# Kernel tuning notes

Hardware: AMD Instinct MI355X
Metric: run time of the kernel (lower is better)

Reference implementation:

```python
import jax, jax.numpy as jnp
import numpy as np

HEADS = 8
HID = 256
D = HID // HEADS
NEG_SLOPE = 0.2  # PyG leaky_relu negative_slope default in HANConv
NA, NPAP, CIN = 10000, 20000, 256
E = 256000
OUT = 16


def seg_softmax(scores, seg, num_segments):
    # scores: [E, H]; softmax over edges sharing the same dst segment id
    m = jax.ops.segment_max(scores, seg, num_segments=num_segments)
    m = jnp.where(jnp.isfinite(m), m, 0.0)
    e = jnp.exp(scores - m[seg])
    s = jax.ops.segment_sum(e, seg, num_segments=num_segments)
    return e / (s[seg] + 1e-16)


def han_edge(h_src, h_dst, att_src, att_dst, src, dst, num_dst):
    # h_src: [Ns, H, D]; att_*: [H, D]; src/dst: [E]
    a = (h_src * att_src).sum(-1)[src] + (h_dst * att_dst).sum(-1)[dst]  # [E, H]
    alpha = seg_softmax(jax.nn.leaky_relu(a, NEG_SLOPE), dst, num_dst)
    out = jax.ops.segment_sum(h_src[src] * alpha[..., None], dst, num_segments=num_dst)
    return jax.nn.relu(out.reshape(num_dst, HID))


def semantic_group(xs, q, k_W, k_b):
    out = jnp.stack(xs)                                            # [M, N, F]
    score = (jnp.tanh(out @ k_W + k_b) * q).sum(-1).mean(axis=1)   # [M]
    attn = jax.nn.softmax(score)                                   # softmax over metapaths
    return (out * attn[:, None, None]).sum(0)                      # [N, F]


def setup_inputs() -> dict:
    key = jax.random.key(0)
    ks = jax.random.split(key, 32)
    n = lambda i, shape, s: jax.random.normal(ks[i], shape, dtype=jnp.float32) * s
    ri = lambda i, hi: jax.random.randint(ks[i], (E,), 0, hi).astype(jnp.int64)
    w_scale = (1.0 / CIN) ** 0.5
    return {
        "x_author": n(0, (NA, CIN), 1.0),
        "x_paper": n(1, (NPAP, CIN), 1.0),
        "W_author": n(2, (CIN, HID), w_scale),
        "b_author": jnp.zeros((HID,), jnp.float32),
        "W_paper": n(3, (CIN, HID), w_scale),
        "b_paper": jnp.zeros((HID,), jnp.float32),
        "att_sw": n(4, (HEADS, D), 0.1),
        "att_dw": n(5, (HEADS, D), 0.1),
        "att_sc": n(6, (HEADS, D), 0.1),
        "att_dc": n(7, (HEADS, D), 0.1),
        "att_sr": n(8, (HEADS, D), 0.1),
        "att_dr": n(9, (HEADS, D), 0.1),
        "k_W": n(10, (HID, HID), (1.0 / HID) ** 0.5),
        "k_b": jnp.zeros((HID,), jnp.float32),
        "q": n(11, (HID,), 0.1),
        "lin_W": n(12, (HID, OUT), (1.0 / HID) ** 0.5),
        "lin_b": jnp.zeros((OUT,), jnp.float32),
        "ew_src": ri(13, NA), "ew_dst": ri(14, NPAP),
        "ec_src": ri(15, NPAP), "ec_dst": ri(16, NPAP),
        "er_src": ri(17, NPAP), "er_dst": ri(18, NA),
    }


def reference(x_author, x_paper, W_author, b_author, W_paper, b_paper,
              att_sw, att_dw, att_sc, att_dc, att_sr, att_dr,
              k_W, k_b, q, lin_W, lin_b,
              ew_src, ew_dst, ec_src, ec_dst, er_src, er_dst):
    # per-node-type projection -> [N, H, D]
    h_a = (x_author @ W_author + b_author).reshape(NA, HEADS, D)
    h_p = (x_paper @ W_paper + b_paper).reshape(NPAP, HEADS, D)
    # per-edge-type gather / attention / segment-softmax / scatter
    o_writes = han_edge(h_a, h_p, att_sw, att_dw, ew_src, ew_dst, NPAP)  # author->paper
    o_cites = han_edge(h_p, h_p, att_sc, att_dc, ec_src, ec_dst, NPAP)   # paper->paper
    o_rev = han_edge(h_p, h_a, att_sr, att_dr, er_src, er_dst, NA)       # paper->author
    # semantic-level attention over metapaths per dst node type
    paper_out = semantic_group([o_writes, o_cites], q, k_W, k_b)
    author_out = semantic_group([o_rev], q, k_W, k_b)
    # global_add_pool per node type (batch=None -> single graph) + shared linear
    pooled = jnp.stack([author_out.sum(0), paper_out.sum(0)])  # [2, HID]
    return pooled @ lin_W + lin_b                              # [2, OUT]
```

## Files before the change

### kernel.cpp

```cpp
#include <hip/hip_runtime.h>
#include <hip/hip_bf16.h>

#define HEADS 8
#define HID 256
#define NA 10000
#define NPAP 20000
#define NE 256000
#define N_SEG (2 * NPAP + NA)
#define TOTE (3 * NE)
#define NEG_SLOPE 0.2f

typedef __attribute__((ext_vector_type(8))) short bf16x8;
typedef __attribute__((ext_vector_type(4))) float f32x4;

__device__ __forceinline__ short f2bf(float x) {
    unsigned u = __float_as_uint(x);
    unsigned r = (u + 0x7fffu + ((u >> 16) & 1u)) >> 16;
    return (short)r;
}
__device__ __forceinline__ float bf2f(short s) {
    return __uint_as_float(((unsigned)(unsigned short)s) << 16);
}
__device__ __forceinline__ float bflo(unsigned u) { return __uint_as_float(u << 16); }
__device__ __forceinline__ float bfhi(unsigned u) { return __uint_as_float(u & 0xffff0000u); }

#define W_BLKS 48
#define DEG_BLKS 3000
__global__ __launch_bounds__(256) void prep(
    const float* __restrict__ W_a, short* __restrict__ WaT,
    const float* __restrict__ W_p, short* __restrict__ WpT,
    const float* __restrict__ k_W, short* __restrict__ kWT,
    const int* __restrict__ ewd, const int* __restrict__ ecd, const int* __restrict__ erd,
    int* __restrict__ deg4, unsigned short* __restrict__ rank16)
{
    __shared__ short T[64][65];
    int b = blockIdx.x;
    int t = threadIdx.x;
    if (b < W_BLKS) {
        int z = b >> 4, rem = b & 15;
        int k0 = (rem & 3) * 64, c0 = (rem >> 2) * 64;
        const float* W = z == 0 ? W_a : (z == 1 ? W_p : k_W);
        short* Wt      = z == 0 ? WaT : (z == 1 ? WpT : kWT);
        int rr = t >> 6, c = t & 63;
#pragma unroll
        for (int p = 0; p < 16; ++p) {
            int r = rr + p * 4;
            T[c][r] = f2bf(W[(size_t)(k0 + r) * 256 + c0 + c]);
        }
        __syncthreads();
#pragma unroll
        for (int p = 0; p < 16; ++p) {
            int cc = rr + p * 4;
            Wt[(size_t)(c0 + cc) * 256 + k0 + c] = T[cc][c];
        }
    } else {
        int bb = b - W_BLKS;
        int e = bb * 256 + t;
        if (e >= TOTE) return;
        int d;
        if (e < NE)          d = ewd[e];
        else if (e < 2 * NE) d = ecd[e - NE] + NPAP;
        else                 d = erd[e - 2 * NE] + 2 * NPAP;
        int r = atomicAdd(&deg4[(bb & 3) * N_SEG + d], 1);
        rank16[e] = (unsigned short)r;
    }
}

__global__ __launch_bounds__(256) void proj_gemm(
    const float* __restrict__ A0, const short* __restrict__ Wt0, const float* __restrict__ b0,
    short* __restrict__ C0, unsigned char* __restrict__ H80, int N0, int nb0,
    const float* __restrict__ A1, const short* __restrict__ Wt1, const float* __restrict__ b1,
    short* __restrict__ C1, unsigned char* __restrict__ H81, int N1)
{
    __shared__ short As[64][64];
    __shared__ short Ws[256][64];

    int bx = blockIdx.x;
    const float* A; const short* Wt; const float* bias; short* Cb; unsigned char* H8; int N, row0;
    if (bx < nb0) { A = A0; Wt = Wt0; bias = b0; Cb = C0; H8 = H80; N = N0; row0 = bx * 64; }
    else          { A = A1; Wt = Wt1; bias = b1; Cb = C1; H8 = H81; N = N1; row0 = (bx - nb0) * 64; }

    int tid = threadIdx.x;
    int w = tid >> 6, l = tid & 63;
    int lr = l & 15, lh = l >> 4;
    int swz = (l & 7) << 3;

    f32x4 acc[4][4] = {};

    for (int k0 = 0; k0 < 256; k0 += 64) {
#pragma unroll
        for (int i = 0; i < 4; ++i) {
            int lin = tid + i * 256;
            int r = lin >> 4, fc = (lin & 15) << 2;
            float4 v = make_float4(0.f, 0.f, 0.f, 0.f);
            int gr = row0 + r;
            if (gr < N) v = *reinterpret_cast<const float4*>(&A[(size_t)gr * 256 + k0 + fc]);
            short4 o;
            o.x = f2bf(v.x); o.y = f2bf(v.y); o.z = f2bf(v.z); o.w = f2bf(v.w);
            *reinterpret_cast<short4*>(&As[r][fc ^ ((r & 7) << 3)]) = o;
        }
#pragma unroll
        for (int i = 0; i < 8; ++i) {
            int lin = tid + i * 256;
            int c = lin >> 3, kc = (lin & 7) << 3;
            *reinterpret_cast<bf16x8*>(&Ws[c][kc ^ ((c & 7) << 3)]) =
                *reinterpret_cast<const bf16x8*>(&Wt[(size_t)c * 256 + k0 + kc]);
        }
        __syncthreads();
#pragma unroll
        for (int kk = 0; kk < 64; kk += 32) {
            int krow = (kk + lh * 8) ^ swz;
            bf16x8 af[4], bfr[4];
#pragma unroll
            for (int mi = 0; mi < 4; ++mi)
                af[mi] = *reinterpret_cast<bf16x8*>(&As[mi * 16 + lr][krow]);
#pragma unroll
            for (int ni = 0; ni < 4; ++ni)
                bfr[ni] = *reinterpret_cast<bf16x8*>(&Ws[w * 64 + ni * 16 + lr][krow]);
#pragma unroll
            for (int mi = 0; mi < 4; ++mi)
#pragma unroll
                for (int ni = 0; ni < 4; ++ni)
                    acc[mi][ni] = __builtin_amdgcn_mfma_f32_16x16x32_bf16(
                        af[mi], bfr[ni], acc[mi][ni], 0, 0, 0);
        }
        __syncthreads();
    }

#pragma unroll
    for (int mi = 0; mi < 4; ++mi) {
        int rb = row0 + mi * 16 + lh * 4;
#pragma unroll
        for (int ni = 0; ni < 4; ++ni) {
            int c = w * 64 + ni * 16 + lr;
            float bc = bias[c];
#pragma unroll
            for (int j = 0; j < 4; ++j) {
                if (rb + j < N) {
                    float v = acc[mi][ni][j] + bc;
                    Cb[(size_t)(rb + j) * 256 + c] = f2bf(v);
                    unsigned pk = __builtin_amdgcn_cvt_pk_fp8_f32(v, v, 0, false);
                    H8[(size_t)(rb + j) * 256 + c] = (unsigned char)pk;
                }
            }
        }
    }
}

__global__ __launch_bounds__(256) void gemm_score(
    const short* __restrict__ A0, const short* __restrict__ Wt, const float* __restrict__ kb,
    float* __restrict__ sAcc0, int N0, int nb0,
    const short* __restrict__ A1, float* __restrict__ sAcc1, int N1,
    const float* __restrict__ q)
{
    __shared__ short As[64][64];
    __shared__ short Ws[256][64];
    __shared__ float red[256];

    int bx = blockIdx.x;
    const short* A; float* sAcc; int N, row0;
    if (bx < nb0) { A = A0; sAcc = sAcc0; N = N0; row0 = bx * 64; }
    else          { A = A1; sAcc = sAcc1; N = N1; row0 = (bx - nb0) * 64; }

    int tid = threadIdx.x;
    int w = tid >> 6, l = tid & 63;
    int lr = l & 15, lh = l >> 4;
    int swz = (l & 7) << 3;

    f32x4 acc[4][4] = {};

    for (int k0 = 0; k0 < 256; k0 += 64) {
#pragma unroll
        for (int i = 0; i < 2; ++i) {
            int lin = tid + i * 256;
            int r = lin >> 3, kc = (lin & 7) << 3;
            bf16x8 v = {};
            int gr = row0 + r;
            if (gr < N) v = *reinterpret_cast<const bf16x8*>(&A[(size_t)gr * 256 + k0 + kc]);
            *reinterpret_cast<bf16x8*>(&As[r][kc ^ ((r & 7) << 3)]) = v;
        }
#pragma unroll
        for (int i = 0; i < 8; ++i) {
            int lin = tid + i * 256;
            int c = lin >> 3, kc = (lin & 7) << 3;
            *reinterpret_cast<bf16x8*>(&Ws[c][kc ^ ((c & 7) << 3)]) =
                *reinterpret_cast<const bf16x8*>(&Wt[(size_t)c * 256 + k0 + kc]);
        }
        __syncthreads();
#pragma unroll
        for (int kk = 0; kk < 64; kk += 32) {
            int krow = (kk + lh * 8) ^ swz;
            bf16x8 af[4], bfr[4];
#pragma unroll
            for (int mi = 0; mi < 4; ++mi)
                af[mi] = *reinterpret_cast<bf16x8*>(&As[mi * 16 + lr][krow]);
#pragma unroll
            for (int ni = 0; ni < 4; ++ni)
                bfr[ni] = *reinterpret_cast<bf16x8*>(&Ws[w * 64 + ni * 16 + lr][krow]);
#pragma unroll
            for (int mi = 0; mi < 4; ++mi)
#pragma unroll
                for (int ni = 0; ni < 4; ++ni)
                    acc[mi][ni] = __builtin_amdgcn_mfma_f32_16x16x32_bf16(
                        af[mi], bfr[ni], acc[mi][ni], 0, 0, 0);
        }
        __syncthreads();
    }

    float s = 0.f;
#pragma unroll
    for (int mi = 0; mi < 4; ++mi) {
        int rb = row0 + mi * 16 + lh * 4;
#pragma unroll
        for (int ni = 0; ni < 4; ++ni) {
            int c = w * 64 + ni * 16 + lr;
            float bc = kb[c], qc = q[c];
#pragma unroll
            for (int j = 0; j < 4; ++j) {
                if (rb + j < N) s += tanhf(acc[mi][ni][j] + bc) * qc;
            }
        }
    }
    red[tid] = s;
    __syncthreads();
    for (int k = 128; k > 0; k >>= 1) {
        if (tid < k) red[tid] += red[tid + k];
        __syncthreads();
    }
    if (tid == 0) atomicAdd(sAcc, red[0]);
}

__global__ __launch_bounds__(256) void node_att_all(
    const short* __restrict__ h_p, const short* __restrict__ h_a,
    const float* __restrict__ att_dw, const float* __restrict__ att_sc,
    const float* __restrict__ att_dc, const float* __restrict__ att_sr,
    const float* __restrict__ att_sw, const float* __restrict__ att_dr,
    float* __restrict__ a_dw, float* __restrict__ a_sc,
    float* __restrict__ a_dc, float* __restrict__ a_sr,
    float* __restrict__ a_sw, float* __restrict__ a_dr)
{
    int n = blockIdx.x;
    int t = threadIdx.x;
    if (n < NPAP) {
        float v = bf2f(h_p[(size_t)n * 256 + t]);
        float d0 = v * att_dw[t], d1 = v * att_sc[t], d2 = v * att_dc[t], d3 = v * att_sr[t];
#pragma unroll
        for (int k = 16; k > 0; k >>= 1) {
            d0 += __shfl_xor(d0, k, 64);
            d1 += __shfl_xor(d1, k, 64);
            d2 += __shfl_xor(d2, k, 64);
            d3 += __shfl_xor(d3, k, 64);
        }
        if ((t & 31) == 0) {
            int hh = t >> 5;
            a_dw[n * 8 + hh] = d0; a_sc[n * 8 + hh] = d1;
            a_dc[n * 8 + hh] = d2; a_sr[n * 8 + hh] = d3;
        }
    } else {
        int m = n - NPAP;
        float v = bf2f(h_a[(size_t)m * 256 + t]);
        float d0 = v * att_sw[t], d1 = v * att_dr[t];
#pragma unroll
        for (int k = 16; k > 0; k >>= 1) {
            d0 += __shfl_xor(d0, k, 64);
            d1 += __shfl_xor(d1, k, 64);
        }
        if ((t & 31) == 0) {
            int hh = t >> 5;
            a_sw[m * 8 + hh] = d0; a_dr[m * 8 + hh] = d1;
        }
    }
}

__global__ void scan_l1(const int* __restrict__ deg4, int* __restrict__ excl,
                        int* __restrict__ bsum, int N)
{
    __shared__ int buf[256];
    int t = threadIdx.x;
    int base = blockIdx.x * 256;
    int idx = base + t;
    int v = 0;
    if (idx < N)
        v = deg4[idx] + deg4[N_SEG + idx] + deg4[2 * N_SEG + idx] + deg4[3 * N_SEG + idx];
    buf[t] = v;
    __syncthreads();
    for (int off = 1; off < 256; off <<= 1) {
        int add = (t >= off) ? buf[t - off] : 0;
        __syncthreads();
        buf[t] += add;
        __syncthreads();
    }
    if (idx < N) excl[idx] = buf[t] - v;
    if (t == 255) bsum[blockIdx.x] = buf[255];
}

__global__ void scan_l2(const int* __restrict__ bsum, int* __restrict__ boff, int nb)
{
    __shared__ int buf[256];
    int t = threadIdx.x;
    int v = (t < nb) ? bsum[t] : 0;
    buf[t] = v;
    __syncthreads();
    for (int off = 1; off < 256; off <<= 1) {
        int add = (t >= off) ? buf[t - off] : 0;
        __syncthreads();
        buf[t] += add;
        __syncthreads();
    }
    if (t < nb) boff[t] = buf[t] - v;
}

__global__ void scan_l3(const int* __restrict__ excl, const int* __restrict__ boff,
                        const int* __restrict__ deg4,
                        int* __restrict__ starts, int* __restrict__ base4, int N)
{
    int i = blockIdx.x * 256 + threadIdx.x;
    if (i > N) return;
    int v = (i == N) ? TOTE : excl[i] + boff[i >> 8];
    starts[i] = v;
    if (i < N) {
        int c = v;
        base4[i] = c;                 c += deg4[i];
        base4[N_SEG + i] = c;         c += deg4[N_SEG + i];
        base4[2 * N_SEG + i] = c;     c += deg4[2 * N_SEG + i];
        base4[3 * N_SEG + i] = c;
    }
}

__global__ __launch_bounds__(256) void scatter_edges(
    const int* __restrict__ ews, const int* __restrict__ ewd,
    const int* __restrict__ ecs, const int* __restrict__ ecd,
    const int* __restrict__ ers, const int* __restrict__ erd,
    const int* __restrict__ base4, const unsigned short* __restrict__ rank16,
    int* __restrict__ ssrc)
{
    int e = blockIdx.x * 256 + threadIdx.x;
    if (e >= TOTE) return;
    int s, d;
    if (e < NE)          { s = ews[e];          d = ewd[e]; }
    else if (e < 2 * NE) { s = ecs[e - NE];     d = ecd[e - NE] + NPAP; }
    else                 { s = ers[e - 2 * NE]; d = erd[e - 2 * NE] + 2 * NPAP; }
    int shadow = (e >> 8) & 3;
    int pos = base4[shadow * N_SEG + d] + (int)rank16[e];
    ssrc[pos] = s;
}

__global__ __launch_bounds__(256) void han_seg(
    const int* __restrict__ starts, const int* __restrict__ ssrc,
    const float* __restrict__ a_sw, const float* __restrict__ a_dw,
    const float* __restrict__ a_sc, const float* __restrict__ a_dc,
    const float* __restrict__ a_sr, const float* __restrict__ a_dr,
    const unsigned* __restrict__ h8_a, const unsigned* __restrict__ h8_p,
    short* __restrict__ outall)
{
    int w = threadIdx.x >> 6, lane = threadIdx.x & 63;
    int n = blockIdx.x * 4 + w;
    if (n >= N_SEG) return;

    const float* asrc; const float* adst; const unsigned* h8;
    int nloc;
    if (n < NPAP)          { nloc = n;            asrc = a_sw; adst = a_dw; h8 = h8_a; }
    else if (n < 2 * NPAP) { nloc = n - NPAP;     asrc = a_sc; adst = a_dc; h8 = h8_p; }
    else                   { nloc = n - 2 * NPAP; asrc = a_sr; adst = a_dr; h8 = h8_p; }

    int hh = lane >> 3;
    int c0 = lane << 2;
    float ad = adst[nloc * 8 + hh];

    int i = starts[n], end = starts[n + 1];
    float ac0 = 0.f, ac1 = 0.f, ac2 = 0.f, ac3 = 0.f, ps = 0.f;

    for (; i + 4 <= end; i += 4) {
        int s0 = __builtin_amdgcn_readfirstlane(ssrc[i]);
        int s1 = __builtin_amdgcn_readfirstlane(ssrc[i + 1]);
        int s2 = __builtin_amdgcn_readfirstlane(ssrc[i + 2]);
        int s3 = __builtin_amdgcn_readfirstlane(ssrc[i + 3]);
        float x0 = asrc[s0 * 8 + hh] + ad;
        float x1 = asrc[s1 * 8 + hh] + ad;
        float x2 = asrc[s2 * 8 + hh] + ad;
        float x3 = asrc[s3 * 8 + hh] + ad;
        unsigned v0 = h8[s0 * 64 + lane];
        unsigned v1 = h8[s1 * 64 + lane];
        unsigned v2 = h8[s2 * 64 + lane];
        unsigned v3 = h8[s3 * 64 + lane];
        x0 = x0 > 0.f ? x0 : NEG_SLOPE * x0;
        x1 = x1 > 0.f ? x1 : NEG_SLOPE * x1;
        x2 = x2 > 0.f ? x2 : NEG_SLOPE * x2;
        x3 = x3 > 0.f ? x3 : NEG_SLOPE * x3;
        float e0 = __expf(x0), e1 = __expf(x1), e2 = __expf(x2), e3 = __expf(x3);
        ps += (e0 + e1) + (e2 + e3);
        ac0 += e0 * __builtin_amdgcn_cvt_f32_fp8(v0, 0) + e1 * __builtin_amdgcn_cvt_f32_fp8(v1, 0)
             + e2 * __builtin_amdgcn_cvt_f32_fp8(v2, 0) + e3 * __builtin_amdgcn_cvt_f32_fp8(v3, 0);
        ac1 += e0 * __builtin_amdgcn_cvt_f32_fp8(v0, 1) + e1 * __builtin_amdgcn_cvt_f32_fp8(v1, 1)
             + e2 * __builtin_amdgcn_cvt_f32_fp8(v2, 1) + e3 * __builtin_amdgcn_cvt_f32_fp8(v3, 1);
        ac2 += e0 * __builtin_amdgcn_cvt_f32_fp8(v0, 2) + e1 * __builtin_amdgcn_cvt_f32_fp8(v1, 2)
             + e2 * __builtin_amdgcn_cvt_f32_fp8(v2, 2) + e3 * __builtin_amdgcn_cvt_f32_fp8(v3, 2);
        ac3 += e0 * __builtin_amdgcn_cvt_f32_fp8(v0, 3) + e1 * __builtin_amdgcn_cvt_f32_fp8(v1, 3)
             + e2 * __builtin_amdgcn_cvt_f32_fp8(v2, 3) + e3 * __builtin_amdgcn_cvt_f32_fp8(v3, 3);
    }
    for (; i < end; ++i) {
        int s0 = __builtin_amdgcn_readfirstlane(ssrc[i]);
        float x0 = asrc[s0 * 8 + hh] + ad;
        unsigned v0 = h8[s0 * 64 + lane];
        x0 = x0 > 0.f ? x0 : NEG_SLOPE * x0;
        float e0 = __expf(x0);
        ps += e0;
        ac0 += e0 * __builtin_amdgcn_cvt_f32_fp8(v0, 0);
        ac1 += e0 * __builtin_amdgcn_cvt_f32_fp8(v0, 1);
        ac2 += e0 * __builtin_amdgcn_cvt_f32_fp8(v0, 2);
        ac3 += e0 * __builtin_amdgcn_cvt_f32_fp8(v0, 3);
    }

    float inv = 1.0f / (ps + 1e-16f);
    float o0 = ac0 * inv, o1 = ac1 * inv, o2 = ac2 * inv, o3 = ac3 * inv;
    short4 o;
    o.x = f2bf(o0 > 0.f ? o0 : 0.f);
    o.y = f2bf(o1 > 0.f ? o1 : 0.f);
    o.z = f2bf(o2 > 0.f ? o2 : 0.f);
    o.w = f2bf(o3 > 0.f ? o3 : 0.f);
    *reinterpret_cast<short4*>(&outall[(size_t)n * 256 + c0]) = o;
}

__global__ void colsum3(const short* __restrict__ outall,
                        float* __restrict__ cw, float* __restrict__ cc,
                        float* __restrict__ cr)
{
    int t = threadIdx.x;
    int r0 = blockIdx.x * 32;
    int rend = r0 + 32 < N_SEG ? r0 + 32 : N_SEG;
    float s = 0.f;
    for (int r = r0; r < rend; ++r) s += bf2f(outall[(size_t)r * 256 + t]);
    float* cs = r0 < NPAP ? cw : (r0 < 2 * NPAP ? cc : cr);
    atomicAdd(&cs[t], s);
}

__global__ void finalize(const float* __restrict__ scoreAcc,
                         const float* __restrict__ colsum_w, const float* __restrict__ colsum_c,
                         const float* __restrict__ colsum_r,
                         const float* __restrict__ lin_W, const float* __restrict__ lin_b,
                         float* __restrict__ out)
{
    int t = threadIdx.x;
    if (t >= 32) return;
    float sw = scoreAcc[0] / (float)NPAP;
    float scs = scoreAcc[1] / (float)NPAP;
    float mx = fmaxf(sw, scs);
    float ew = expf(sw - mx), ec = expf(scs - mx);
    float aw = ew / (ew + ec), ac = ec / (ew + ec);
    int row = t >> 4, j = t & 15;
    float acc = lin_b[j];
    for (int c = 0; c < 256; ++c) {
        float p = (row == 0) ? colsum_r[c] : (aw * colsum_w[c] + ac * colsum_c[c]);
        acc += p * lin_W[c * 16 + j];
    }
    out[row * 16 + j] = acc;
}

extern "C" void kernel_launch(void* const* d_in, const int* in_sizes, int n_in,
                              void* d_out, int out_size, void* d_ws, size_t ws_size,
                              hipStream_t stream)
{
    const float* x_a   = (const float*)d_in[0];
    const float* x_p   = (const float*)d_in[1];
    const float* W_a   = (const float*)d_in[2];
    const float* b_a   = (const float*)d_in[3];
    const float* W_p   = (const float*)d_in[4];
    const float* b_p   = (const float*)d_in[5];
    const float* att_sw = (const float*)d_in[6];
    const float* att_dw = (const float*)d_in[7];
    const float* att_sc = (const float*)d_in[8];
    const float* att_dc = (const float*)d_in[9];
    const float* att_sr = (const float*)d_in[10];
    const float* att_dr = (const float*)d_in[11];
    const float* k_W   = (const float*)d_in[12];
    const float* k_b   = (const float*)d_in[13];
    const float* q     = (const float*)d_in[14];
    const float* lin_W = (const float*)d_in[15];
    const float* lin_b = (const float*)d_in[16];
    const int* ew_src = (const int*)d_in[17];
    const int* ew_dst = (const int*)d_in[18];
    const int* ec_src = (const int*)d_in[19];
    const int* ec_dst = (const int*)d_in[20];
    const int* er_src = (const int*)d_in[21];
    const int* er_dst = (const int*)d_in[22];

    float* ws = (float*)d_ws;
    size_t off = 0;
    auto align4 = [&]() { off = (off + 3) & ~(size_t)3; };

    short* h_a_bf = (short*)(ws + off); off += (size_t)NA * HID / 2;
    short* h_p_bf = (short*)(ws + off); off += (size_t)NPAP * HID / 2;
    unsigned char* h8_a = (unsigned char*)(ws + off); off += (size_t)NA * HID / 4;
    unsigned char* h8_p = (unsigned char*)(ws + off); off += (size_t)NPAP * HID / 4;
    short* WaT  = (short*)(ws + off); off += 256 * 256 / 2;
    short* WpT  = (short*)(ws + off); off += 256 * 256 / 2;
    short* kWT  = (short*)(ws + off); off += 256 * 256 / 2;
    float* a_sw = ws + off; off += (size_t)NA * 8;
    float* a_dw = ws + off; off += (size_t)NPAP * 8;
    float* a_sc = ws + off; off += (size_t)NPAP * 8;
    float* a_dc = ws + off; off += (size_t)NPAP * 8;
    float* a_sr = ws + off; off += (size_t)NPAP * 8;
    float* a_dr = ws + off; off += (size_t)NA * 8;
    short* outall = (short*)(ws + off); off += (size_t)N_SEG * HID / 2;
    int* starts  = (int*)(ws + off); off += N_SEG + 1; align4();
    int* base4   = (int*)(ws + off); off += 4 * N_SEG; align4();
    int* sexcl   = (int*)(ws + off); off += N_SEG + 1; align4();
    int* sbsum   = (int*)(ws + off); off += 256;
    int* sboff   = (int*)(ws + off); off += 256;
    int* ssrc    = (int*)(ws + off); off += TOTE;
    unsigned short* rank16 = (unsigned short*)(ws + off); off += TOTE / 2;
    size_t zero_start = off;
    int* deg4       = (int*)(ws + off); off += 4 * N_SEG; align4();
    float* colsum_w = ws + off; off += 256;
    float* colsum_c = ws + off; off += 256;
    float* colsum_r = ws + off; off += 256;
    float* score    = ws + off; off += 2;
    size_t zero_bytes = (off - zero_start) * sizeof(float);

    hipMemsetAsync(ws + zero_start, 0, zero_bytes, stream);

    prep<<<W_BLKS + DEG_BLKS, 256, 0, stream>>>(
        W_a, WaT, W_p, WpT, k_W, kWT, ew_dst, ec_dst, er_dst, deg4, rank16);

    const int nbA = (NA + 63) / 64, nbP = (NPAP + 63) / 64;
    proj_gemm<<<nbA + nbP, 256, 0, stream>>>(
        x_a, WaT, b_a, h_a_bf, h8_a, NA, nbA,
        x_p, WpT, b_p, h_p_bf, h8_p, NPAP);

    node_att_all<<<NPAP + NA, 256, 0, stream>>>(
        h_p_bf, h_a_bf, att_dw, att_sc, att_dc, att_sr, att_sw, att_dr,
        a_dw, a_sc, a_dc, a_sr, a_sw, a_dr);

    const int nbS = (N_SEG + 255) / 256;
    scan_l1<<<nbS, 256, 0, stream>>>(deg4, sexcl, sbsum, N_SEG);
    scan_l2<<<1, 256, 0, stream>>>(sbsum, sboff, nbS);
    scan_l3<<<(N_SEG + 1 + 255) / 256, 256, 0, stream>>>(sexcl, sboff, deg4, starts, base4, N_SEG);
    scatter_edges<<<(TOTE + 255) / 256, 256, 0, stream>>>(ew_src, ew_dst, ec_src, ec_dst,
                                                          er_src, er_dst, base4, rank16, ssrc);

    han_seg<<<(N_SEG + 3) / 4, 256, 0, stream>>>(starts, ssrc, a_sw, a_dw, a_sc, a_dc, a_sr, a_dr,
                                                 (const unsigned*)h8_a, (const unsigned*)h8_p,
                                                 outall);

    colsum3<<<(N_SEG + 31) / 32, 256, 0, stream>>>(outall, colsum_w, colsum_c, colsum_r);
    gemm_score<<<2 * nbP, 256, 0, stream>>>(
        outall, kWT, k_b, score + 0, NPAP, nbP,
        outall + (size_t)NPAP * HID, score + 1, NPAP, q);

    finalize<<<1, 64, 0, stream>>>(score, colsum_w, colsum_c, colsum_r, lin_W, lin_b, (float*)d_out);
}
```

Measured before the change: 239.1 us.

## Merge independent kernels to cut launch count across the pipeline

Regroups the kernel sequence so independent work shares one launch: the degree counting now rides with the projection GEMM, the first scan level with the node attention dot products, and the column sums with the semantic score GEMM. The weight conversion becomes its own small kernel. The aim is fewer launches and inter-kernel gaps, while adding branch divergence between block types and extra shared memory held by the scan and colsum blocks.

```diff
diff --git a/kernel.cpp b/kernel.cpp
--- a/kernel.cpp
+++ b/kernel.cpp
@@ -9,6 +9,14 @@
 #define N_SEG (2 * NPAP + NA)
 #define TOTE (3 * NE)
 #define NEG_SLOPE 0.2f
+#define NBA 157
+#define NBP 313
+#define PROJ_BLKS (NBA + NBP)
+#define DEG_BLKS 3000
+#define NATT_BLKS (NPAP + NA)
+#define NBS ((N_SEG + 255) / 256)
+#define SCORE_BLKS (2 * NBP)
+#define COLSUM_BLKS ((N_SEG + 31) / 32)
 
 typedef __attribute__((ext_vector_type(8))) short bf16x8;
 typedef __attribute__((ext_vector_type(4))) float f32x4;
@@ -21,40 +29,49 @@
 __device__ __forceinline__ float bf2f(short s) {
     return __uint_as_float(((unsigned)(unsigned short)s) << 16);
 }
-__device__ __forceinline__ float bflo(unsigned u) { return __uint_as_float(u << 16); }
-__device__ __forceinline__ float bfhi(unsigned u) { return __uint_as_float(u & 0xffff0000u); }
-
-#define W_BLKS 48
-#define DEG_BLKS 3000
-__global__ __launch_bounds__(256) void prep(
+
+__global__ __launch_bounds__(256) void wconv(
     const float* __restrict__ W_a, short* __restrict__ WaT,
     const float* __restrict__ W_p, short* __restrict__ WpT,
-    const float* __restrict__ k_W, short* __restrict__ kWT,
-    const int* __restrict__ ewd, const int* __restrict__ ecd, const int* __restrict__ erd,
-    int* __restrict__ deg4, unsigned short* __restrict__ rank16)
+    const float* __restrict__ k_W, short* __restrict__ kWT)
 {
     __shared__ short T[64][65];
     int b = blockIdx.x;
     int t = threadIdx.x;
-    if (b < W_BLKS) {
-        int z = b >> 4, rem = b & 15;
-        int k0 = (rem & 3) * 64, c0 = (rem >> 2) * 64;
-        const float* W = z == 0 ? W_a : (z == 1 ? W_p : k_W);
-        short* Wt      = z == 0 ? WaT : (z == 1 ? WpT : kWT);
-        int rr = t >> 6, c = t & 63;
-#pragma unroll
-        for (int p = 0; p < 16; ++p) {
-            int r = rr + p * 4;
-            T[c][r] = f2bf(W[(size_t)(k0 + r) * 256 + c0 + c]);
-        }
-        __syncthreads();
-#pragma unroll
-        for (int p = 0; p < 16; ++p) {
-            int cc = rr + p * 4;
-            Wt[(size_t)(c0 + cc) * 256 + k0 + c] = T[cc][c];
-        }
-    } else {
-        int bb = b - W_BLKS;
+    int z = b >> 4, rem = b & 15;
+    int k0 = (rem & 3) * 64, c0 = (rem >> 2) * 64;
+    const float* W = z == 0 ? W_a : (z == 1 ? W_p : k_W);
+    short* Wt      = z == 0 ? WaT : (z == 1 ? WpT : kWT);
+    int rr = t >> 6, c = t & 63;
+#pragma unroll
+    for (int p = 0; p < 16; ++p) {
+        int r = rr + p * 4;
+        T[c][r] = f2bf(W[(size_t)(k0 + r) * 256 + c0 + c]);
+    }
+    __syncthreads();
+#pragma unroll
+    for (int p = 0; p < 16; ++p) {
+        int cc = rr + p * 4;
+        Wt[(size_t)(c0 + cc) * 256 + k0 + c] = T[cc][c];
+    }
+}
+
+__global__ __launch_bounds__(256) void proj_deg(
+    const float* __restrict__ A0, const short* __restrict__ Wt0, const float* __restrict__ b0,
+    short* __restrict__ C0, unsigned char* __restrict__ H80,
+    const float* __restrict__ A1, const short* __restrict__ Wt1, const float* __restrict__ b1,
+    short* __restrict__ C1, unsigned char* __restrict__ H81,
+    const int* __restrict__ ewd, const int* __restrict__ ecd, const int* __restrict__ erd,
+    int* __restrict__ deg4, unsigned short* __restrict__ rank16)
+{
+    __shared__ short As[64][64];
+    __shared__ short Ws[256][64];
+
+    int b = blockIdx.x;
+    int t = threadIdx.x;
+
+    if (b >= PROJ_BLKS) {
+        int bb = b - PROJ_BLKS;
         int e = bb * 256 + t;
         if (e >= TOTE) return;
         int d;
@@ -63,25 +80,14 @@
         else                 d = erd[e - 2 * NE] + 2 * NPAP;
         int r = atomicAdd(&deg4[(bb & 3) * N_SEG + d], 1);
         rank16[e] = (unsigned short)r;
-    }
-}
-
-__global__ __launch_bounds__(256) void proj_gemm(
-    const float* __restrict__ A0, const short* __restrict__ Wt0, const float* __restrict__ b0,
-    short* __restrict__ C0, unsigned char* __restrict__ H80, int N0, int nb0,
-    const float* __restrict__ A1, const short* __restrict__ Wt1, const float* __restrict__ b1,
-    short* __restrict__ C1, unsigned char* __restrict__ H81, int N1)
-{
-    __shared__ short As[64][64];
-    __shared__ short Ws[256][64];
-
-    int bx = blockIdx.x;
+        return;
+    }
+
     const float* A; const short* Wt; const float* bias; short* Cb; unsigned char* H8; int N, row0;
-    if (bx < nb0) { A = A0; Wt = Wt0; bias = b0; Cb = C0; H8 = H80; N = N0; row0 = bx * 64; }
-    else          { A = A1; Wt = Wt1; bias = b1; Cb = C1; H8 = H81; N = N1; row0 = (bx - nb0) * 64; }
-
-    int tid = threadIdx.x;
-    int w = tid >> 6, l = tid & 63;
+    if (b < NBA) { A = A0; Wt = Wt0; bias = b0; Cb = C0; H8 = H80; N = NA;   row0 = b * 64; }
+    else         { A = A1; Wt = Wt1; bias = b1; Cb = C1; H8 = H81; N = NPAP; row0 = (b - NBA) * 64; }
+
+    int w = t >> 6, l = t & 63;
     int lr = l & 15, lh = l >> 4;
     int swz = (l & 7) << 3;
 
@@ -90,7 +96,7 @@
     for (int k0 = 0; k0 < 256; k0 += 64) {
 #pragma unroll
         for (int i = 0; i < 4; ++i) {
-            int lin = tid + i * 256;
+            int lin = t + i * 256;
             int r = lin >> 4, fc = (lin & 15) << 2;
             float4 v = make_float4(0.f, 0.f, 0.f, 0.f);
             int gr = row0 + r;
@@ -101,7 +107,7 @@
         }
 #pragma unroll
         for (int i = 0; i < 8; ++i) {
-            int lin = tid + i * 256;
+            int lin = t + i * 256;
             int c = lin >> 3, kc = (lin & 7) << 3;
             *reinterpret_cast<bf16x8*>(&Ws[c][kc ^ ((c & 7) << 3)]) =
                 *reinterpret_cast<const bf16x8*>(&Wt[(size_t)c * 256 + k0 + kc]);
@@ -147,102 +153,41 @@
     }
 }
 
-__global__ __launch_bounds__(256) void gemm_score(
-    const short* __restrict__ A0, const short* __restrict__ Wt, const float* __restrict__ kb,
-    float* __restrict__ sAcc0, int N0, int nb0,
-    const short* __restrict__ A1, float* __restrict__ sAcc1, int N1,
-    const float* __restrict__ q)
-{
-    __shared__ short As[64][64];
-    __shared__ short Ws[256][64];
-    __shared__ float red[256];
-
-    int bx = blockIdx.x;
-    const short* A; float* sAcc; int N, row0;
-    if (bx < nb0) { A = A0; sAcc = sAcc0; N = N0; row0 = bx * 64; }
-    else          { A = A1; sAcc = sAcc1; N = N1; row0 = (bx - nb0) * 64; }
-
-    int tid = threadIdx.x;
-    int w = tid >> 6, l = tid & 63;
-    int lr = l & 15, lh = l >> 4;
-    int swz = (l & 7) << 3;
-
-    f32x4 acc[4][4] = {};
-
-    for (int k0 = 0; k0 < 256; k0 += 64) {
-#pragma unroll
-        for (int i = 0; i < 2; ++i) {
-            int lin = tid + i * 256;
-            int r = lin >> 3, kc = (lin & 7) << 3;
-            bf16x8 v = {};
-            int gr = row0 + r;
-            if (gr < N) v = *reinterpret_cast<const bf16x8*>(&A[(size_t)gr * 256 + k0 + kc]);
-            *reinterpret_cast<bf16x8*>(&As[r][kc ^ ((r & 7) << 3)]) = v;
-        }
-#pragma unroll
-        for (int i = 0; i < 8; ++i) {
-            int lin = tid + i * 256;
-            int c = lin >> 3, kc = (lin & 7) << 3;
-            *reinterpret_cast<bf16x8*>(&Ws[c][kc ^ ((c & 7) << 3)]) =
-                *reinterpret_cast<const bf16x8*>(&Wt[(size_t)c * 256 + k0 + kc]);
-        }
-        __syncthreads();
-#pragma unroll
-        for (int kk = 0; kk < 64; kk += 32) {
-            int krow = (kk + lh * 8) ^ swz;
-            bf16x8 af[4], bfr[4];
-#pragma unroll
-            for (int mi = 0; mi < 4; ++mi)
-                af[mi] = *reinterpret_cast<bf16x8*>(&As[mi * 16 + lr][krow]);
-#pragma unroll
-            for (int ni = 0; ni < 4; ++ni)
-                bfr[ni] = *reinterpret_cast<bf16x8*>(&Ws[w * 64 + ni * 16 + lr][krow]);
-#pragma unroll
-            for (int mi = 0; mi < 4; ++mi)
-#pragma unroll
-                for (int ni = 0; ni < 4; ++ni)
-                    acc[mi][ni] = __builtin_amdgcn_mfma_f32_16x16x32_bf16(
-                        af[mi], bfr[ni], acc[mi][ni], 0, 0, 0);
-        }
-        __syncthreads();
-    }
-
-    float s = 0.f;
-#pragma unroll
-    for (int mi = 0; mi < 4; ++mi) {
-        int rb = row0 + mi * 16 + lh * 4;
-#pragma unroll
-        for (int ni = 0; ni < 4; ++ni) {
-            int c = w * 64 + ni * 16 + lr;
-            float bc = kb[c], qc = q[c];
-#pragma unroll
-            for (int j = 0; j < 4; ++j) {
-                if (rb + j < N) s += tanhf(acc[mi][ni][j] + bc) * qc;
-            }
-        }
-    }
-    red[tid] = s;
-    __syncthreads();
-    for (int k = 128; k > 0; k >>= 1) {
-        if (tid < k) red[tid] += red[tid + k];
-        __syncthreads();
-    }
-    if (tid == 0) atomicAdd(sAcc, red[0]);
-}
-
-__global__ __launch_bounds__(256) void node_att_all(
+__global__ __launch_bounds__(256) void natt_scan(
     const short* __restrict__ h_p, const short* __restrict__ h_a,
     const float* __restrict__ att_dw, const float* __restrict__ att_sc,
     const float* __restrict__ att_dc, const float* __restrict__ att_sr,
     const float* __restrict__ att_sw, const float* __restrict__ att_dr,
     float* __restrict__ a_dw, float* __restrict__ a_sc,
     float* __restrict__ a_dc, float* __restrict__ a_sr,
-    float* __restrict__ a_sw, float* __restrict__ a_dr)
-{
-    int n = blockIdx.x;
+    float* __restrict__ a_sw, float* __restrict__ a_dr,
+    const int* __restrict__ deg4, int* __restrict__ excl, int* __restrict__ bsum)
+{
+    int b = blockIdx.x;
     int t = threadIdx.x;
-    if (n < NPAP) {
-        float v = bf2f(h_p[(size_t)n * 256 + t]);
+
+    if (b >= NATT_BLKS) {
+        __shared__ int buf[256];
+        int bb = b - NATT_BLKS;
+        int idx = bb * 256 + t;
+        int v = 0;
+        if (idx < N_SEG)
+            v = deg4[idx] + deg4[N_SEG + idx] + deg4[2 * N_SEG + idx] + deg4[3 * N_SEG + idx];
+        buf[t] = v;
+        __syncthreads();
+        for (int off = 1; off < 256; off <<= 1) {
+            int add = (t >= off) ? buf[t - off] : 0;
+            __syncthreads();
+            buf[t] += add;
+            __syncthreads();
+        }
+        if (idx < N_SEG) excl[idx] = buf[t] - v;
+        if (t == 255) bsum[bb] = buf[255];
+        return;
+    }
+
+    if (b < NPAP) {
+        float v = bf2f(h_p[(size_t)b * 256 + t]);
         float d0 = v * att_dw[t], d1 = v * att_sc[t], d2 = v * att_dc[t], d3 = v * att_sr[t];
 #pragma unroll
         for (int k = 16; k > 0; k >>= 1) {
@@ -253,11 +198,11 @@
         }
         if ((t & 31) == 0) {
             int hh = t >> 5;
-            a_dw[n * 8 + hh] = d0; a_sc[n * 8 + hh] = d1;
-            a_dc[n * 8 + hh] = d2; a_sr[n * 8 + hh] = d3;
+            a_dw[b * 8 + hh] = d0; a_sc[b * 8 + hh] = d1;
+            a_dc[b * 8 + hh] = d2; a_sr[b * 8 + hh] = d3;
         }
     } else {
-        int m = n - NPAP;
+        int m = b - NPAP;
         float v = bf2f(h_a[(size_t)m * 256 + t]);
         float d0 = v * att_sw[t], d1 = v * att_dr[t];
 #pragma unroll
@@ -270,28 +215,6 @@
             a_sw[m * 8 + hh] = d0; a_dr[m * 8 + hh] = d1;
         }
     }
-}
-
-__global__ void scan_l1(const int* __restrict__ deg4, int* __restrict__ excl,
-                        int* __restrict__ bsum, int N)
-{
-    __shared__ int buf[256];
-    int t = threadIdx.x;
-    int base = blockIdx.x * 256;
-    int idx = base + t;
-    int v = 0;
-    if (idx < N)
-        v = deg4[idx] + deg4[N_SEG + idx] + deg4[2 * N_SEG + idx] + deg4[3 * N_SEG + idx];
-    buf[t] = v;
-    __syncthreads();
-    for (int off = 1; off < 256; off <<= 1) {
-        int add = (t >= off) ? buf[t - off] : 0;
-        __syncthreads();
-        buf[t] += add;
-        __syncthreads();
-    }
-    if (idx < N) excl[idx] = buf[t] - v;
-    if (t == 255) bsum[blockIdx.x] = buf[255];
 }
 
 __global__ void scan_l2(const int* __restrict__ bsum, int* __restrict__ boff, int nb)
@@ -421,17 +344,99 @@
     *reinterpret_cast<short4*>(&outall[(size_t)n * 256 + c0]) = o;
 }
 
-__global__ void colsum3(const short* __restrict__ outall,
-                        float* __restrict__ cw, float* __restrict__ cc,
-                        float* __restrict__ cr)
-{
+__global__ __launch_bounds__(256) void score_colsum(
+    const short* __restrict__ outall, const short* __restrict__ Wt,
+    const float* __restrict__ kb, const float* __restrict__ q,
+    float* __restrict__ score, float* __restrict__ cw, float* __restrict__ cc,
+    float* __restrict__ cr)
+{
+    __shared__ short As[64][64];
+    __shared__ short Ws[256][64];
+    __shared__ float red[256];
+
+    int b = blockIdx.x;
     int t = threadIdx.x;
-    int r0 = blockIdx.x * 32;
-    int rend = r0 + 32 < N_SEG ? r0 + 32 : N_SEG;
+
+    if (b >= SCORE_BLKS) {
+        int r0 = (b - SCORE_BLKS) * 32;
+        int rend = r0 + 32 < N_SEG ? r0 + 32 : N_SEG;
+        float s = 0.f;
+        for (int r = r0; r < rend; ++r) s += bf2f(outall[(size_t)r * 256 + t]);
+        float* cs = r0 < NPAP ? cw : (r0 < 2 * NPAP ? cc : cr);
+        atomicAdd(&cs[t], s);
+        return;
+    }
+
+    const short* A; float* sAcc; int row0;
+    if (b < NBP) { A = outall;                           sAcc = score + 0; row0 = b * 64; }
+    else         { A = outall + (size_t)NPAP * HID;      sAcc = score + 1; row0 = (b - NBP) * 64; }
+    const int N = NPAP;
+
+    int w = t >> 6, l = t & 63;
+    int lr = l & 15, lh = l >> 4;
+    int swz = (l & 7) << 3;
+
+    f32x4 acc[4][4] = {};
+
+    for (int k0 = 0; k0 < 256; k0 += 64) {
+#pragma unroll
+        for (int i = 0; i < 2; ++i) {
+            int lin = t + i * 256;
+            int r = lin >> 3, kc = (lin & 7) << 3;
+            bf16x8 v = {};
+            int gr = row0 + r;
+            if (gr < N) v = *reinterpret_cast<const bf16x8*>(&A[(size_t)gr * 256 + k0 + kc]);
+            *reinterpret_cast<bf16x8*>(&As[r][kc ^ ((r & 7) << 3)]) = v;
+        }
+#pragma unroll
+        for (int i = 0; i < 8; ++i) {
+            int lin = t + i * 256;
+            int c = lin >> 3, kc = (lin & 7) << 3;
+            *reinterpret_cast<bf16x8*>(&Ws[c][kc ^ ((c & 7) << 3)]) =
+                *reinterpret_cast<const bf16x8*>(&Wt[(size_t)c * 256 + k0 + kc]);
+        }
+        __syncthreads();
+#pragma unroll
+        for (int kk = 0; kk < 64; kk += 32) {
+            int krow = (kk + lh * 8) ^ swz;
+            bf16x8 af[4], bfr[4];
+#pragma unroll
+            for (int mi = 0; mi < 4; ++mi)
+                af[mi] = *reinterpret_cast<bf16x8*>(&As[mi * 16 + lr][krow]);
+#pragma unroll
+            for (int ni = 0; ni < 4; ++ni)
+                bfr[ni] = *reinterpret_cast<bf16x8*>(&Ws[w * 64 + ni * 16 + lr][krow]);
+#pragma unroll
+            for (int mi = 0; mi < 4; ++mi)
+#pragma unroll
+                for (int ni = 0; ni < 4; ++ni)
+                    acc[mi][ni] = __builtin_amdgcn_mfma_f32_16x16x32_bf16(
+                        af[mi], bfr[ni], acc[mi][ni], 0, 0, 0);
+        }
+        __syncthreads();
+    }
+
     float s = 0.f;
-    for (int r = r0; r < rend; ++r) s += bf2f(outall[(size_t)r * 256 + t]);
-    float* cs = r0 < NPAP ? cw : (r0 < 2 * NPAP ? cc : cr);
-    atomicAdd(&cs[t], s);
+#pragma unroll
+    for (int mi = 0; mi < 4; ++mi) {
+        int rb = row0 + mi * 16 + lh * 4;
+#pragma unroll
+        for (int ni = 0; ni < 4; ++ni) {
+            int c = w * 64 + ni * 16 + lr;
+            float bc = kb[c], qc = q[c];
+#pragma unroll
+            for (int j = 0; j < 4; ++j) {
+                if (rb + j < N) s += tanhf(acc[mi][ni][j] + bc) * qc;
+            }
+        }
+    }
+    red[t] = s;
+    __syncthreads();
+    for (int k = 128; k > 0; k >>= 1) {
+        if (t < k) red[t] += red[t + k];
+        __syncthreads();
+    }
+    if (t == 0) atomicAdd(sAcc, red[0]);
 }
 
 __global__ void finalize(const float* __restrict__ scoreAcc,
@@ -519,22 +524,21 @@
 
     hipMemsetAsync(ws + zero_start, 0, zero_bytes, stream);
 
-    prep<<<W_BLKS + DEG_BLKS, 256, 0, stream>>>(
-        W_a, WaT, W_p, WpT, k_W, kWT, ew_dst, ec_dst, er_dst, deg4, rank16);
-
-    const int nbA = (NA + 63) / 64, nbP = (NPAP + 63) / 64;
-    proj_gemm<<<nbA + nbP, 256, 0, stream>>>(
-        x_a, WaT, b_a, h_a_bf, h8_a, NA, nbA,
-        x_p, WpT, b_p, h_p_bf, h8_p, NPAP);
-
-    node_att_all<<<NPAP + NA, 256, 0, stream>>>(
+    wconv<<<48, 256, 0, stream>>>(W_a, WaT, W_p, WpT, k_W, kWT);
+
+    proj_deg<<<PROJ_BLKS + DEG_BLKS, 256, 0, stream>>>(
+        x_a, WaT, b_a, h_a_bf, h8_a,
+        x_p, WpT, b_p, h_p_bf, h8_p,
+        ew_dst, ec_dst, er_dst, deg4, rank16);
+
+    natt_scan<<<NATT_BLKS + NBS, 256, 0, stream>>>(
         h_p_bf, h_a_bf, att_dw, att_sc, att_dc, att_sr, att_sw, att_dr,
-        a_dw, a_sc, a_dc, a_sr, a_sw, a_dr);
-
-    const int nbS = (N_SEG + 255) / 256;
-    scan_l1<<<nbS, 256, 0, stream>>>(deg4, sexcl, sbsum, N_SEG);
-    scan_l2<<<1, 256, 0, stream>>>(sbsum, sboff, nbS);
+        a_dw, a_sc, a_dc, a_sr, a_sw, a_dr,
+        deg4, sexcl, sbsum);
+
+    scan_l2<<<1, 256, 0, stream>>>(sbsum, sboff, NBS);
     scan_l3<<<(N_SEG + 1 + 255) / 256, 256, 0, stream>>>(sexcl, sboff, deg4, starts, base4, N_SEG);
+
     scatter_edges<<<(TOTE + 255) / 256, 256, 0, stream>>>(ew_src, ew_dst, ec_src, ec_dst,
                                                           er_src, er_dst, base4, rank16, ssrc);
 
@@ -542,10 +546,8 @@
                                                  (const unsigned*)h8_a, (const unsigned*)h8_p,
                                                  outall);
 
-    colsum3<<<(N_SEG + 31) / 32, 256, 0, stream>>>(outall, colsum_w, colsum_c, colsum_r);
-    gemm_score<<<2 * nbP, 256, 0, stream>>>(
-        outall, kWT, k_b, score + 0, NPAP, nbP,
-        outall + (size_t)NPAP * HID, score + 1, NPAP, q);
+    score_colsum<<<SCORE_BLKS + COLSUM_BLKS, 256, 0, stream>>>(
+        outall, kWT, k_b, q, score, colsum_w, colsum_c, colsum_r);
 
     finalize<<<1, 64, 0, stream>>>(score, colsum_w, colsum_c, colsum_r, lin_W, lin_b, (float*)d_out);
 }
```

After: 233.6 us. 1.02x faster.
